# Optimization experiments

Hardware: AMD Instinct MI355X
Metric: run time of the kernel (lower is better)

Reference implementation:

```python
import jax, jax.numpy as jnp
import numpy as np

N_NODES = 50000
N_EDGES = 800000
N_GRAPHS = 2000
N_PAIRS = 4096
IN_CH = 64
EMB = 128
HID = 256
OUT = 1


def gcn_conv(x, edge_index, W, b):
    # PyG GCNConv: h = x @ W^T, then D^{-1/2}(A+I)D^{-1/2} h + b
    h = x @ W.T                                  # [N, out]
    row, col = edge_index[0], edge_index[1]
    ones = jnp.ones((edge_index.shape[1],), h.dtype)
    deg = jax.ops.segment_sum(ones, col, num_segments=N_NODES) + 1.0  # self-loop
    dinv = jax.lax.rsqrt(deg)
    norm = dinv[row] * dinv[col]                 # [E]
    agg = jax.ops.segment_sum(h[row] * norm[:, None], col, num_segments=N_NODES)
    agg = agg + h * (1.0 / deg)[:, None]         # self-loop term (dinv[i]^2)
    return agg + b


def setup_inputs() -> dict:
    key = jax.random.key(0)
    ks = jax.random.split(key, 10)
    x = jax.random.normal(ks[0], (N_NODES, IN_CH), jnp.float32)
    edge_index = jax.random.randint(ks[1], (2, N_EDGES), 0, N_NODES, jnp.int64)
    batch = jnp.sort(jax.random.randint(ks[2], (N_NODES,), 0, N_GRAPHS, jnp.int64))
    drug_drug_batch = jax.random.randint(ks[3], (2, N_PAIRS), 0, N_GRAPHS, jnp.int64)

    def xavier(k, shape):
        fan_out, fan_in = shape
        lim = jnp.sqrt(6.0 / (fan_in + fan_out))
        return jax.random.uniform(k, shape, jnp.float32, -lim, lim)

    return {
        "x": x, "edge_index": edge_index, "batch": batch,
        "drug_drug_batch": drug_drug_batch,
        "conv1_w": xavier(ks[4], (EMB, IN_CH)), "conv1_b": jnp.zeros((EMB,), jnp.float32),
        "conv2_w": xavier(ks[5], (EMB, EMB)), "conv2_b": jnp.zeros((EMB,), jnp.float32),
        "reg1_w": xavier(ks[6], (HID, 2 * EMB)), "reg1_b": jnp.zeros((HID,), jnp.float32),
        "reg2_w": xavier(ks[7], (OUT, HID)), "reg2_b": jnp.zeros((OUT,), jnp.float32),
    }


def reference(x, edge_index, batch, drug_drug_batch,
              conv1_w, conv1_b, conv2_w, conv2_b,
              reg1_w, reg1_b, reg2_w, reg2_b):
    h = jax.nn.relu(gcn_conv(x, edge_index, conv1_w, conv1_b))
    h = jax.nn.relu(gcn_conv(h, edge_index, conv2_w, conv2_b))

    # scatter_mean readout over graphs
    gsum = jax.ops.segment_sum(h, batch, num_segments=N_GRAPHS)
    cnt = jax.ops.segment_sum(jnp.ones((N_NODES,), h.dtype), batch, num_segments=N_GRAPHS)
    graph_embeds = gsum / jnp.maximum(cnt, 1.0)[:, None]

    # quantize drug ids to dense graph indices (np.digitize on unique+1, as in source)
    dd = np.asarray(drug_drug_batch)
    bins = np.unique(dd.flatten()) + 1
    q = jnp.asarray(np.digitize(dd, bins))       # [2, P]

    pairs = jnp.concatenate([graph_embeds[q[0]], graph_embeds[q[1]]], axis=1)  # [P, 2*EMB]
    out = jax.nn.relu(pairs @ reg1_w.T + reg1_b)
    return out @ reg2_w.T + reg2_b
```

## Files before the change

### kernel.cpp

```cpp
#include <hip/hip_runtime.h>

#define N_NODES  50000
#define N_PAD    50048
#define N_EDGES  800000
#define N_GRAPHS 2000
#define N_PAIRS  4096
#define IN_CH    64
#define EMB      128
#define HID      256
#define PPB      16

__global__ void k_pre(const int* __restrict__ col, const int* __restrict__ batch,
                      const float* __restrict__ w1, const float* __restrict__ w2,
                      int* __restrict__ deg, int* __restrict__ pos_e, int* __restrict__ cnt,
                      float* __restrict__ wt1, float* __restrict__ wt2) {
    int e = blockIdx.x * 256 + threadIdx.x;
    if (e < N_EDGES) {
        int c = col[e];
        pos_e[e] = atomicAdd(&deg[c], 1);
    }
    if (e < N_NODES) atomicAdd(&cnt[batch[e]], 1);
    if (e < EMB * IN_CH) {
        int j = e / IN_CH, k = e % IN_CH;
        wt1[k * EMB + j] = w1[e];
    } else if (e < EMB * IN_CH + EMB * EMB) {
        int t = e - EMB * IN_CH;
        int j = t / EMB, k = t % EMB;
        wt2[k * EMB + j] = w2[t];
    }
}

__device__ inline int wave_incl_scan(int x, int lane) {
    #pragma unroll
    for (int off = 1; off < 64; off <<= 1) {
        int y = __shfl_up(x, off, 64);
        if (lane >= off) x += y;
    }
    return x;
}

__global__ void k_scan1(const int* __restrict__ in, int* __restrict__ part, int n) {
    __shared__ int ws[4];
    int i = blockIdx.x * 256 + threadIdx.x;
    int lane = threadIdx.x & 63, wid = threadIdx.x >> 6;
    int v = (i < n) ? in[i] : 0;
    int x = wave_incl_scan(v, lane);
    if (lane == 63) ws[wid] = x;
    __syncthreads();
    if (threadIdx.x == 0) part[blockIdx.x] = ws[0] + ws[1] + ws[2] + ws[3];
}

__global__ void k_scan2(int* __restrict__ part, int nb) {
    __shared__ int ws[4];
    int t = threadIdx.x, lane = t & 63, wid = t >> 6;
    int v = (t < nb) ? part[t] : 0;
    int x = wave_incl_scan(v, lane);
    if (lane == 63) ws[wid] = x;
    __syncthreads();
    int add = 0;
    for (int w = 0; w < wid; ++w) add += ws[w];
    if (t < nb) part[t] = x - v + add;
}

__global__ void k_scan3d(const int* __restrict__ in, const int* __restrict__ part,
                         int* __restrict__ off, float* __restrict__ dinv) {
    __shared__ int ws[4];
    int i = blockIdx.x * 256 + threadIdx.x;
    int lane = threadIdx.x & 63, wid = threadIdx.x >> 6;
    int v = (i < N_NODES) ? in[i] : 0;
    int x = wave_incl_scan(v, lane);
    if (lane == 63) ws[wid] = x;
    __syncthreads();
    int add = part[blockIdx.x];
    for (int w = 0; w < wid; ++w) add += ws[w];
    if (i < N_NODES) {
        off[i] = x - v + add;
        dinv[i] = 1.0f / sqrtf((float)(v + 1));
    }
    if (i == 0) off[N_NODES] = N_EDGES;
}

__global__ void k_fill_scale(const int* __restrict__ row, const int* __restrict__ col,
                             const int* __restrict__ pos_e, const int* __restrict__ off,
                             int* __restrict__ csr_row,
                             const float4* __restrict__ x, const float* __restrict__ dinv,
                             float4* __restrict__ xs) {
    int idx = blockIdx.x * 256 + threadIdx.x;
    if (idx < N_EDGES) {
        int c = col[idx];
        int p = pos_e[idx];
        csr_row[off[c] + p] = row[idx];
    } else {
        int i = idx - N_EDGES;
        int n = i >> 4;
        float d = dinv[n];
        float4 v = x[i];
        v.x *= d; v.y *= d; v.z *= d; v.w *= d;
        xs[i] = v;
    }
}

__device__ inline void f4add(float4& a, const float4 b) {
    a.x += b.x; a.y += b.y; a.z += b.z; a.w += b.w;
}

template <int C>
__global__ void k_gather8(const float4* __restrict__ hs, const int* __restrict__ csr_row,
                          const int* __restrict__ off, const float* __restrict__ dinv,
                          float4* __restrict__ out) {
    constexpr int L = C / 4;
    constexpr int NPB = 256 / L;
    int local = threadIdx.x / L;
    int c4 = threadIdx.x % L;
    int n = blockIdx.x * NPB + local;
    int s = off[n], e = off[n + 1];
    float4 acc = hs[n * L + c4];
    int i = s;
    for (; i + 8 <= e; i += 8) {
        int r0 = csr_row[i + 0], r1 = csr_row[i + 1], r2 = csr_row[i + 2], r3 = csr_row[i + 3];
        int r4 = csr_row[i + 4], r5 = csr_row[i + 5], r6 = csr_row[i + 6], r7 = csr_row[i + 7];
        float4 a0 = hs[r0 * L + c4], a1 = hs[r1 * L + c4];
        float4 a2 = hs[r2 * L + c4], a3 = hs[r3 * L + c4];
        float4 a4 = hs[r4 * L + c4], a5 = hs[r5 * L + c4];
        float4 a6 = hs[r6 * L + c4], a7 = hs[r7 * L + c4];
        f4add(a0, a1); f4add(a2, a3); f4add(a4, a5); f4add(a6, a7);
        f4add(a0, a2); f4add(a4, a6);
        f4add(a0, a4);
        f4add(acc, a0);
    }
    for (; i < e; ++i) {
        int r = csr_row[i];
        float4 a = hs[r * L + c4];
        f4add(acc, a);
    }
    float dn = dinv[n];
    acc.x *= dn; acc.y *= dn; acc.z *= dn; acc.w *= dn;
    out[n * L + c4] = acc;
}

__global__ void k_gather_ro(const float4* __restrict__ t2, const int* __restrict__ csr_row,
                            const int* __restrict__ off, const float* __restrict__ dinv,
                            const float* __restrict__ bias, const int* __restrict__ batch,
                            float* __restrict__ gsum) {
    constexpr int L = EMB / 4;
    constexpr int NPB = 8;
    __shared__ __align__(16) float hb[NPB][EMB];
    __shared__ int bg[NPB];
    int local = threadIdx.x >> 5;
    int c4 = threadIdx.x & 31;
    int n0 = blockIdx.x * NPB;
    int n = n0 + local;
    if (threadIdx.x < NPB) bg[threadIdx.x] = batch[n0 + threadIdx.x];
    int s = off[n], e = off[n + 1];
    float4 acc = t2[n * L + c4];
    int i = s;
    for (; i + 8 <= e; i += 8) {
        int r0 = csr_row[i + 0], r1 = csr_row[i + 1], r2 = csr_row[i + 2], r3 = csr_row[i + 3];
        int r4 = csr_row[i + 4], r5 = csr_row[i + 5], r6 = csr_row[i + 6], r7 = csr_row[i + 7];
        float4 a0 = t2[r0 * L + c4], a1 = t2[r1 * L + c4];
        float4 a2 = t2[r2 * L + c4], a3 = t2[r3 * L + c4];
        float4 a4 = t2[r4 * L + c4], a5 = t2[r5 * L + c4];
        float4 a6 = t2[r6 * L + c4], a7 = t2[r7 * L + c4];
        f4add(a0, a1); f4add(a2, a3); f4add(a4, a5); f4add(a6, a7);
        f4add(a0, a2); f4add(a4, a6);
        f4add(a0, a4);
        f4add(acc, a0);
    }
    for (; i < e; ++i) {
        int r = csr_row[i];
        float4 a = t2[r * L + c4];
        f4add(acc, a);
    }
    float dn = dinv[n];
    float4 b = reinterpret_cast<const float4*>(bias)[c4];
    acc.x = fmaxf(fmaf(acc.x, dn, b.x), 0.f);
    acc.y = fmaxf(fmaf(acc.y, dn, b.y), 0.f);
    acc.z = fmaxf(fmaf(acc.z, dn, b.z), 0.f);
    acc.w = fmaxf(fmaf(acc.w, dn, b.w), 0.f);
    *reinterpret_cast<float4*>(&hb[local][c4 * 4]) = acc;
    __syncthreads();
    int ch = threadIdx.x;
    if (ch < EMB) {
        int g = bg[0];
        float a = 0.f;
        #pragma unroll
        for (int j = 0; j < NPB; ++j) {
            int gj = bg[j];
            if (gj != g) { atomicAdd(&gsum[g * EMB + ch], a); a = 0.f; g = gj; }
            a += hb[j][ch];
        }
        atomicAdd(&gsum[g * EMB + ch], a);
    }
}

template <int K, bool RELU, bool BIAS, bool POSTSCALE>
__global__ void k_gemmv5(const float* __restrict__ A, const float* __restrict__ Wt,
                         const float* __restrict__ bias, const float* __restrict__ rowscale,
                         float* __restrict__ out) {
    __shared__ __align__(16) float a_lds[64 * K];
    int t = threadIdx.x;
    {
        const float4* Ag = reinterpret_cast<const float4*>(A + (size_t)blockIdx.x * 64 * K);
        float4* Al = reinterpret_cast<float4*>(a_lds);
        constexpr int NV = (64 * K) / (4 * 256);
        #pragma unroll
        for (int i = 0; i < NV; ++i) Al[t + i * 256] = Ag[t + i * 256];
    }
    __syncthreads();
    int cq = (t & 31) << 2;
    int rg = t >> 5;
    float4 acc[8];
    #pragma unroll
    for (int r = 0; r < 8; ++r) acc[r] = make_float4(0.f, 0.f, 0.f, 0.f);
    #pragma unroll 2
    for (int k = 0; k < K; k += 4) {
        float4 w0 = *reinterpret_cast<const float4*>(&Wt[(k + 0) * EMB + cq]);
        float4 w1 = *reinterpret_cast<const float4*>(&Wt[(k + 1) * EMB + cq]);
        float4 w2 = *reinterpret_cast<const float4*>(&Wt[(k + 2) * EMB + cq]);
        float4 w3 = *reinterpret_cast<const float4*>(&Wt[(k + 3) * EMB + cq]);
        #pragma unroll
        for (int r = 0; r < 8; ++r) {
            float4 a = *reinterpret_cast<const float4*>(&a_lds[(rg * 8 + r) * K + k]);
            acc[r].x = fmaf(a.x, w0.x, fmaf(a.y, w1.x, fmaf(a.z, w2.x, fmaf(a.w, w3.x, acc[r].x))));
            acc[r].y = fmaf(a.x, w0.y, fmaf(a.y, w1.y, fmaf(a.z, w2.y, fmaf(a.w, w3.y, acc[r].y))));
            acc[r].z = fmaf(a.x, w0.z, fmaf(a.y, w1.z, fmaf(a.z, w2.z, fmaf(a.w, w3.z, acc[r].z))));
            acc[r].w = fmaf(a.x, w0.w, fmaf(a.y, w1.w, fmaf(a.z, w2.w, fmaf(a.w, w3.w, acc[r].w))));
        }
    }
    int row0 = blockIdx.x * 64 + rg * 8;
    #pragma unroll
    for (int r = 0; r < 8; ++r) {
        int row = row0 + r;
        if (row < N_NODES) {
            float4 v = acc[r];
            if (BIAS) {
                float4 b = *reinterpret_cast<const float4*>(&bias[cq]);
                v.x += b.x; v.y += b.y; v.z += b.z; v.w += b.w;
            }
            if (RELU) {
                v.x = fmaxf(v.x, 0.f); v.y = fmaxf(v.y, 0.f);
                v.z = fmaxf(v.z, 0.f); v.w = fmaxf(v.w, 0.f);
            }
            if (POSTSCALE) {
                float sc = rowscale[row];
                v.x *= sc; v.y *= sc; v.z *= sc; v.w *= sc;
            }
            *reinterpret_cast<float4*>(&out[(size_t)row * EMB + cq]) = v;
        }
    }
}

__global__ void k_digitize(const int* __restrict__ dd, int* __restrict__ rankx) {
    __shared__ int pres[N_GRAPHS];
    __shared__ int ws[4];
    __shared__ int carry;
    int t = threadIdx.x, lane = t & 63, wid = t >> 6;
    for (int i = t; i < N_GRAPHS; i += 256) pres[i] = 0;
    __syncthreads();
    for (int i = t; i < 2 * N_PAIRS; i += 256) pres[dd[i]] = 1;
    if (t == 0) carry = 0;
    __syncthreads();
    for (int base = 0; base < N_GRAPHS; base += 256) {
        int i = base + t;
        int v = (i < N_GRAPHS) ? pres[i] : 0;
        int x = wave_incl_scan(v, lane);
        if (lane == 63) ws[wid] = x;
        __syncthreads();
        int add = carry;
        for (int w = 0; w < wid; ++w) add += ws[w];
        if (i < N_GRAPHS) rankx[i] = x - v + add;
        __syncthreads();
        if (t == 255) carry = add + x;
        __syncthreads();
    }
}

__global__ void k_mlp16(const float* __restrict__ gemb, const int* __restrict__ cnt,
                        const int* __restrict__ dd, const int* __restrict__ rankx,
                        const float* __restrict__ w1, const float* __restrict__ b1,
                        const float* __restrict__ w2, const float* __restrict__ b2,
                        float* __restrict__ out) {
    __shared__ __align__(16) float pv[PPB][2 * EMB];
    __shared__ float wpart[4][PPB];
    int p0 = blockIdx.x * PPB;
    int t = threadIdx.x;
    int lane = t & 63, wid = t >> 6;
    #pragma unroll
    for (int j = 0; j < PPB; ++j) {
        int p = p0 + j;
        if (t < EMB) {
            int ga = rankx[dd[p]];
            int ca = cnt[ga];
            float ra = 1.0f / (float)(ca > 1 ? ca : 1);
            pv[j][t] = gemb[ga * EMB + t] * ra;
        } else {
            int gb = rankx[dd[N_PAIRS + p]];
            int cb = cnt[gb];
            float rb = 1.0f / (float)(cb > 1 ? cb : 1);
            pv[j][t] = gemb[gb * EMB + (t - EMB)] * rb;
        }
    }
    __syncthreads();
    float acc[PPB];
    float bv = b1[t];
    #pragma unroll
    for (int j = 0; j < PPB; ++j) acc[j] = bv;
    const float4* wrow = reinterpret_cast<const float4*>(&w1[t * 2 * EMB]);
    for (int k = 0; k < (2 * EMB) / 4; ++k) {
        float4 w = wrow[k];
        #pragma unroll
        for (int j = 0; j < PPB; ++j) {
            const float4 xv = *reinterpret_cast<const float4*>(&pv[j][k * 4]);
            acc[j] = fmaf(xv.x, w.x, fmaf(xv.y, w.y, fmaf(xv.z, w.z, fmaf(xv.w, w.w, acc[j]))));
        }
    }
    float w2t = w2[t];
    float contrib[PPB];
    #pragma unroll
    for (int j = 0; j < PPB; ++j) contrib[j] = fmaxf(acc[j], 0.f) * w2t;
    #pragma unroll
    for (int off = 32; off > 0; off >>= 1) {
        #pragma unroll
        for (int j = 0; j < PPB; ++j) contrib[j] += __shfl_down(contrib[j], off, 64);
    }
    if (lane == 0) {
        #pragma unroll
        for (int j = 0; j < PPB; ++j) wpart[wid][j] = contrib[j];
    }
    __syncthreads();
    if (t < PPB) {
        out[p0 + t] = wpart[0][t] + wpart[1][t] + wpart[2][t] + wpart[3][t] + b2[0];
    }
}

extern "C" void kernel_launch(void* const* d_in, const int* in_sizes, int n_in,
                              void* d_out, int out_size, void* d_ws, size_t ws_size,
                              hipStream_t stream) {
    const float* x        = (const float*)d_in[0];
    const int*   ei       = (const int*)d_in[1];
    const int*   batch    = (const int*)d_in[2];
    const int*   dd       = (const int*)d_in[3];
    const float* conv1_w  = (const float*)d_in[4];
    const float* conv1_b  = (const float*)d_in[5];
    const float* conv2_w  = (const float*)d_in[6];
    const float* conv2_b  = (const float*)d_in[7];
    const float* reg1_w   = (const float*)d_in[8];
    const float* reg1_b   = (const float*)d_in[9];
    const float* reg2_w   = (const float*)d_in[10];
    const float* reg2_b   = (const float*)d_in[11];
    float* outp = (float*)d_out;

    const int* ei_row = ei;
    const int* ei_col = ei + N_EDGES;

    char* ws = (char*)d_ws;
    size_t o = 0;
    auto alloc = [&](size_t bytes) -> void* {
        void* p = ws + o;
        o = (o + bytes + 255) & ~(size_t)255;
        return p;
    };
    size_t zero_start = o;
    int*   deg     = (int*)alloc(N_NODES * 4);
    int*   cnt     = (int*)alloc(N_GRAPHS * 4);
    float* gsum    = (float*)alloc(N_GRAPHS * EMB * 4);
    size_t zero_bytes = o - zero_start;
    int*   off     = (int*)alloc((N_NODES + 1) * 4);
    float* dinv    = (float*)alloc(N_NODES * 4);
    int*   part    = (int*)alloc(256 * 4);
    int*   pos_e   = (int*)alloc(N_EDGES * 4);
    int*   csr_row = (int*)alloc(N_EDGES * 4);
    int*   rankx   = (int*)alloc(N_GRAPHS * 4);
    float* Wt1     = (float*)alloc(IN_CH * EMB * 4);
    float* Wt2     = (float*)alloc(EMB * EMB * 4);
    float* aggx    = (float*)alloc((size_t)N_PAD * IN_CH * 4);
    float* h1s     = (float*)alloc((size_t)N_PAD * EMB * 4);
    float* t2      = (float*)alloc((size_t)N_PAD * EMB * 4);
    float* xs      = t2;

    (void)ws_size; (void)in_sizes; (void)n_in; (void)out_size;

    hipMemsetAsync(ws + zero_start, 0, zero_bytes, stream);

    k_pre<<<N_EDGES / 256, 256, 0, stream>>>(ei_col, batch, conv1_w, conv2_w,
                                             deg, pos_e, cnt, Wt1, Wt2);
    {
        int nb = (N_NODES + 255) / 256;
        k_scan1<<<nb, 256, 0, stream>>>(deg, part, N_NODES);
        k_scan2<<<1, 256, 0, stream>>>(part, nb);
        k_scan3d<<<nb, 256, 0, stream>>>(deg, part, off, dinv);
    }
    k_fill_scale<<<(N_EDGES + N_NODES * (IN_CH / 4)) / 256, 256, 0, stream>>>(
        ei_row, ei_col, pos_e, off, csr_row, (const float4*)x, dinv, (float4*)xs);

    k_gather8<IN_CH><<<N_NODES / (256 / (IN_CH / 4)), 256, 0, stream>>>(
        (const float4*)xs, csr_row, off, dinv, (float4*)aggx);
    k_gemmv5<IN_CH, true, true, true><<<N_PAD / 64, 256, 0, stream>>>(
        aggx, Wt1, conv1_b, dinv, h1s);

    k_gemmv5<EMB, false, false, false><<<N_PAD / 64, 256, 0, stream>>>(
        h1s, Wt2, nullptr, nullptr, t2);
    k_gather_ro<<<N_NODES / 8, 256, 0, stream>>>(
        (const float4*)t2, csr_row, off, dinv, conv2_b, batch, gsum);

    k_digitize<<<1, 256, 0, stream>>>(dd, rankx);

    k_mlp16<<<N_PAIRS / PPB, 256, 0, stream>>>(gsum, cnt, dd, rankx,
                                               reg1_w, reg1_b, reg2_w, reg2_b, outp);
}
```

Before: 238.9 us.

## Fuse conv1 gather into GEMM and split conv2 readout gather into channel halves

Conv1's neighbor aggregation is fused with the 64->128 GEMM in one kernel, so the intermediate aggx buffer is no longer written and re-read. The conv2 gather+readout is split into two launches, each covering 64 of the 128 channels. This halves the per-pass gather working set, likely for better cache hit rates, at the cost of reading the CSR indices twice. The fused kernel uses 32-node tiles with 4 rows per thread, which lowers arithmetic reuse of the weights per block.

```diff
diff --git a/kernel.cpp b/kernel.cpp
--- a/kernel.cpp
+++ b/kernel.cpp
@@ -104,98 +104,87 @@
     a.x += b.x; a.y += b.y; a.z += b.z; a.w += b.w;
 }
 
-template <int C>
-__global__ void k_gather8(const float4* __restrict__ hs, const int* __restrict__ csr_row,
-                          const int* __restrict__ off, const float* __restrict__ dinv,
-                          float4* __restrict__ out) {
-    constexpr int L = C / 4;
-    constexpr int NPB = 256 / L;
-    int local = threadIdx.x / L;
-    int c4 = threadIdx.x % L;
-    int n = blockIdx.x * NPB + local;
-    int s = off[n], e = off[n + 1];
-    float4 acc = hs[n * L + c4];
-    int i = s;
-    for (; i + 8 <= e; i += 8) {
-        int r0 = csr_row[i + 0], r1 = csr_row[i + 1], r2 = csr_row[i + 2], r3 = csr_row[i + 3];
-        int r4 = csr_row[i + 4], r5 = csr_row[i + 5], r6 = csr_row[i + 6], r7 = csr_row[i + 7];
-        float4 a0 = hs[r0 * L + c4], a1 = hs[r1 * L + c4];
-        float4 a2 = hs[r2 * L + c4], a3 = hs[r3 * L + c4];
-        float4 a4 = hs[r4 * L + c4], a5 = hs[r5 * L + c4];
-        float4 a6 = hs[r6 * L + c4], a7 = hs[r7 * L + c4];
-        f4add(a0, a1); f4add(a2, a3); f4add(a4, a5); f4add(a6, a7);
-        f4add(a0, a2); f4add(a4, a6);
-        f4add(a0, a4);
-        f4add(acc, a0);
-    }
-    for (; i < e; ++i) {
-        int r = csr_row[i];
-        float4 a = hs[r * L + c4];
-        f4add(acc, a);
-    }
-    float dn = dinv[n];
-    acc.x *= dn; acc.y *= dn; acc.z *= dn; acc.w *= dn;
-    out[n * L + c4] = acc;
-}
-
-__global__ void k_gather_ro(const float4* __restrict__ t2, const int* __restrict__ csr_row,
-                            const int* __restrict__ off, const float* __restrict__ dinv,
-                            const float* __restrict__ bias, const int* __restrict__ batch,
-                            float* __restrict__ gsum) {
-    constexpr int L = EMB / 4;
-    constexpr int NPB = 8;
-    __shared__ __align__(16) float hb[NPB][EMB];
-    __shared__ int bg[NPB];
-    int local = threadIdx.x >> 5;
-    int c4 = threadIdx.x & 31;
-    int n0 = blockIdx.x * NPB;
-    int n = n0 + local;
-    if (threadIdx.x < NPB) bg[threadIdx.x] = batch[n0 + threadIdx.x];
-    int s = off[n], e = off[n + 1];
-    float4 acc = t2[n * L + c4];
-    int i = s;
-    for (; i + 8 <= e; i += 8) {
-        int r0 = csr_row[i + 0], r1 = csr_row[i + 1], r2 = csr_row[i + 2], r3 = csr_row[i + 3];
-        int r4 = csr_row[i + 4], r5 = csr_row[i + 5], r6 = csr_row[i + 6], r7 = csr_row[i + 7];
-        float4 a0 = t2[r0 * L + c4], a1 = t2[r1 * L + c4];
-        float4 a2 = t2[r2 * L + c4], a3 = t2[r3 * L + c4];
-        float4 a4 = t2[r4 * L + c4], a5 = t2[r5 * L + c4];
-        float4 a6 = t2[r6 * L + c4], a7 = t2[r7 * L + c4];
-        f4add(a0, a1); f4add(a2, a3); f4add(a4, a5); f4add(a6, a7);
-        f4add(a0, a2); f4add(a4, a6);
-        f4add(a0, a4);
-        f4add(acc, a0);
-    }
-    for (; i < e; ++i) {
-        int r = csr_row[i];
-        float4 a = t2[r * L + c4];
-        f4add(acc, a);
-    }
-    float dn = dinv[n];
-    float4 b = reinterpret_cast<const float4*>(bias)[c4];
-    acc.x = fmaxf(fmaf(acc.x, dn, b.x), 0.f);
-    acc.y = fmaxf(fmaf(acc.y, dn, b.y), 0.f);
-    acc.z = fmaxf(fmaf(acc.z, dn, b.z), 0.f);
-    acc.w = fmaxf(fmaf(acc.w, dn, b.w), 0.f);
-    *reinterpret_cast<float4*>(&hb[local][c4 * 4]) = acc;
-    __syncthreads();
-    int ch = threadIdx.x;
-    if (ch < EMB) {
-        int g = bg[0];
-        float a = 0.f;
-        #pragma unroll
-        for (int j = 0; j < NPB; ++j) {
-            int gj = bg[j];
-            if (gj != g) { atomicAdd(&gsum[g * EMB + ch], a); a = 0.f; g = gj; }
-            a += hb[j][ch];
-        }
-        atomicAdd(&gsum[g * EMB + ch], a);
-    }
-}
-
-template <int K, bool RELU, bool BIAS, bool POSTSCALE>
+__global__ __launch_bounds__(256) void k_conv1f(
+        const float4* __restrict__ xs, const int* __restrict__ csr_row,
+        const int* __restrict__ off, const float* __restrict__ dinv,
+        const float* __restrict__ w1t, const float* __restrict__ b1,
+        float* __restrict__ h1s) {
+    __shared__ __align__(16) float a_lds[32 * IN_CH];
+    int t = threadIdx.x;
+    int base = blockIdx.x * 32;
+    {
+        int c4 = t & 15;
+        #pragma unroll
+        for (int g = 0; g < 2; ++g) {
+            int nl = (t >> 4) + g * 16;
+            int n = base + nl;
+            float4 acc = make_float4(0.f, 0.f, 0.f, 0.f);
+            if (n < N_NODES) {
+                int s = off[n], e = off[n + 1];
+                acc = xs[n * 16 + c4];
+                int i = s;
+                for (; i + 8 <= e; i += 8) {
+                    int r0 = csr_row[i + 0], r1 = csr_row[i + 1], r2 = csr_row[i + 2], r3 = csr_row[i + 3];
+                    int r4 = csr_row[i + 4], r5 = csr_row[i + 5], r6 = csr_row[i + 6], r7 = csr_row[i + 7];
+                    float4 a0 = xs[r0 * 16 + c4], a1 = xs[r1 * 16 + c4];
+                    float4 a2 = xs[r2 * 16 + c4], a3 = xs[r3 * 16 + c4];
+                    float4 a4 = xs[r4 * 16 + c4], a5 = xs[r5 * 16 + c4];
+                    float4 a6 = xs[r6 * 16 + c4], a7 = xs[r7 * 16 + c4];
+                    f4add(a0, a1); f4add(a2, a3); f4add(a4, a5); f4add(a6, a7);
+                    f4add(a0, a2); f4add(a4, a6);
+                    f4add(a0, a4);
+                    f4add(acc, a0);
+                }
+                for (; i < e; ++i) {
+                    float4 a = xs[csr_row[i] * 16 + c4];
+                    f4add(acc, a);
+                }
+                float dn = dinv[n];
+                acc.x *= dn; acc.y *= dn; acc.z *= dn; acc.w *= dn;
+            }
+            *reinterpret_cast<float4*>(&a_lds[nl * IN_CH + c4 * 4]) = acc;
+        }
+    }
+    __syncthreads();
+    {
+        int cq = (t & 31) << 2;
+        int rg = t >> 5;
+        float4 acc[4];
+        #pragma unroll
+        for (int r = 0; r < 4; ++r) acc[r] = make_float4(0.f, 0.f, 0.f, 0.f);
+        #pragma unroll 2
+        for (int k = 0; k < IN_CH; k += 4) {
+            float4 w0 = *reinterpret_cast<const float4*>(&w1t[(k + 0) * EMB + cq]);
+            float4 w1 = *reinterpret_cast<const float4*>(&w1t[(k + 1) * EMB + cq]);
+            float4 w2 = *reinterpret_cast<const float4*>(&w1t[(k + 2) * EMB + cq]);
+            float4 w3 = *reinterpret_cast<const float4*>(&w1t[(k + 3) * EMB + cq]);
+            #pragma unroll
+            for (int r = 0; r < 4; ++r) {
+                float4 a = *reinterpret_cast<const float4*>(&a_lds[(rg * 4 + r) * IN_CH + k]);
+                acc[r].x = fmaf(a.x, w0.x, fmaf(a.y, w1.x, fmaf(a.z, w2.x, fmaf(a.w, w3.x, acc[r].x))));
+                acc[r].y = fmaf(a.x, w0.y, fmaf(a.y, w1.y, fmaf(a.z, w2.y, fmaf(a.w, w3.y, acc[r].y))));
+                acc[r].z = fmaf(a.x, w0.z, fmaf(a.y, w1.z, fmaf(a.z, w2.z, fmaf(a.w, w3.z, acc[r].z))));
+                acc[r].w = fmaf(a.x, w0.w, fmaf(a.y, w1.w, fmaf(a.z, w2.w, fmaf(a.w, w3.w, acc[r].w))));
+            }
+        }
+        float4 bv = *reinterpret_cast<const float4*>(&b1[cq]);
+        #pragma unroll
+        for (int r = 0; r < 4; ++r) {
+            int row = base + rg * 4 + r;
+            if (row < N_NODES) {
+                float4 v = acc[r];
+                v.x += bv.x; v.y += bv.y; v.z += bv.z; v.w += bv.w;
+                float sc = dinv[row];
+                v.x = fmaxf(v.x, 0.f) * sc; v.y = fmaxf(v.y, 0.f) * sc;
+                v.z = fmaxf(v.z, 0.f) * sc; v.w = fmaxf(v.w, 0.f) * sc;
+                *reinterpret_cast<float4*>(&h1s[(size_t)row * EMB + cq]) = v;
+            }
+        }
+    }
+}
+
+template <int K>
 __global__ void k_gemmv5(const float* __restrict__ A, const float* __restrict__ Wt,
-                         const float* __restrict__ bias, const float* __restrict__ rowscale,
                          float* __restrict__ out) {
     __shared__ __align__(16) float a_lds[64 * K];
     int t = threadIdx.x;
@@ -232,21 +221,65 @@
     for (int r = 0; r < 8; ++r) {
         int row = row0 + r;
         if (row < N_NODES) {
-            float4 v = acc[r];
-            if (BIAS) {
-                float4 b = *reinterpret_cast<const float4*>(&bias[cq]);
-                v.x += b.x; v.y += b.y; v.z += b.z; v.w += b.w;
-            }
-            if (RELU) {
-                v.x = fmaxf(v.x, 0.f); v.y = fmaxf(v.y, 0.f);
-                v.z = fmaxf(v.z, 0.f); v.w = fmaxf(v.w, 0.f);
-            }
-            if (POSTSCALE) {
-                float sc = rowscale[row];
-                v.x *= sc; v.y *= sc; v.z *= sc; v.w *= sc;
-            }
-            *reinterpret_cast<float4*>(&out[(size_t)row * EMB + cq]) = v;
-        }
+            *reinterpret_cast<float4*>(&out[(size_t)row * EMB + cq]) = acc[r];
+        }
+    }
+}
+
+template <int HALF>
+__global__ void k_gro_h(const float4* __restrict__ t2, const int* __restrict__ csr_row,
+                        const int* __restrict__ off, const float* __restrict__ dinv,
+                        const float* __restrict__ bias, const int* __restrict__ batch,
+                        float* __restrict__ gsum) {
+    constexpr int NPB = 16;
+    __shared__ __align__(16) float hb[NPB][64];
+    __shared__ int bg[NPB];
+    int t = threadIdx.x;
+    int local = t >> 4;
+    int c4 = t & 15;
+    int n0 = blockIdx.x * NPB;
+    int n = n0 + local;
+    if (t < NPB) bg[t] = batch[n0 + t];
+    int s = off[n], e = off[n + 1];
+    const int cidx = HALF * 16 + c4;
+    float4 acc = t2[(size_t)n * 32 + cidx];
+    int i = s;
+    for (; i + 8 <= e; i += 8) {
+        int r0 = csr_row[i + 0], r1 = csr_row[i + 1], r2 = csr_row[i + 2], r3 = csr_row[i + 3];
+        int r4 = csr_row[i + 4], r5 = csr_row[i + 5], r6 = csr_row[i + 6], r7 = csr_row[i + 7];
+        float4 a0 = t2[(size_t)r0 * 32 + cidx], a1 = t2[(size_t)r1 * 32 + cidx];
+        float4 a2 = t2[(size_t)r2 * 32 + cidx], a3 = t2[(size_t)r3 * 32 + cidx];
+        float4 a4 = t2[(size_t)r4 * 32 + cidx], a5 = t2[(size_t)r5 * 32 + cidx];
+        float4 a6 = t2[(size_t)r6 * 32 + cidx], a7 = t2[(size_t)r7 * 32 + cidx];
+        f4add(a0, a1); f4add(a2, a3); f4add(a4, a5); f4add(a6, a7);
+        f4add(a0, a2); f4add(a4, a6);
+        f4add(a0, a4);
+        f4add(acc, a0);
+    }
+    for (; i < e; ++i) {
+        float4 a = t2[(size_t)csr_row[i] * 32 + cidx];
+        f4add(acc, a);
+    }
+    float dn = dinv[n];
+    float4 b = reinterpret_cast<const float4*>(bias)[cidx];
+    acc.x = fmaxf(fmaf(acc.x, dn, b.x), 0.f);
+    acc.y = fmaxf(fmaf(acc.y, dn, b.y), 0.f);
+    acc.z = fmaxf(fmaf(acc.z, dn, b.z), 0.f);
+    acc.w = fmaxf(fmaf(acc.w, dn, b.w), 0.f);
+    *reinterpret_cast<float4*>(&hb[local][c4 * 4]) = acc;
+    __syncthreads();
+    {
+        int ch = t & 63, q = t >> 6;
+        int j0 = q * 4;
+        int g = bg[j0];
+        float a = 0.f;
+        #pragma unroll
+        for (int j = j0; j < j0 + 4; ++j) {
+            int gj = bg[j];
+            if (gj != g) { atomicAdd(&gsum[g * EMB + HALF * 64 + ch], a); a = 0.f; g = gj; }
+            a += hb[j][ch];
+        }
+        atomicAdd(&gsum[g * EMB + HALF * 64 + ch], a);
     }
 }
 
@@ -373,7 +406,6 @@
     int*   rankx   = (int*)alloc(N_GRAPHS * 4);
     float* Wt1     = (float*)alloc(IN_CH * EMB * 4);
     float* Wt2     = (float*)alloc(EMB * EMB * 4);
-    float* aggx    = (float*)alloc((size_t)N_PAD * IN_CH * 4);
     float* h1s     = (float*)alloc((size_t)N_PAD * EMB * 4);
     float* t2      = (float*)alloc((size_t)N_PAD * EMB * 4);
     float* xs      = t2;
@@ -393,14 +425,13 @@
     k_fill_scale<<<(N_EDGES + N_NODES * (IN_CH / 4)) / 256, 256, 0, stream>>>(
         ei_row, ei_col, pos_e, off, csr_row, (const float4*)x, dinv, (float4*)xs);
 
-    k_gather8<IN_CH><<<N_NODES / (256 / (IN_CH / 4)), 256, 0, stream>>>(
-        (const float4*)xs, csr_row, off, dinv, (float4*)aggx);
-    k_gemmv5<IN_CH, true, true, true><<<N_PAD / 64, 256, 0, stream>>>(
-        aggx, Wt1, conv1_b, dinv, h1s);
-
-    k_gemmv5<EMB, false, false, false><<<N_PAD / 64, 256, 0, stream>>>(
-        h1s, Wt2, nullptr, nullptr, t2);
-    k_gather_ro<<<N_NODES / 8, 256, 0, stream>>>(
+    k_conv1f<<<N_PAD / 32, 256, 0, stream>>>(
+        (const float4*)xs, csr_row, off, dinv, Wt1, conv1_b, h1s);
+
+    k_gemmv5<EMB><<<N_PAD / 64, 256, 0, stream>>>(h1s, Wt2, t2);
+    k_gro_h<0><<<N_NODES / 16, 256, 0, stream>>>(
+        (const float4*)t2, csr_row, off, dinv, conv2_b, batch, gsum);
+    k_gro_h<1><<<N_NODES / 16, 256, 0, stream>>>(
         (const float4*)t2, csr_row, off, dinv, conv2_b, batch, gsum);
 
     k_digitize<<<1, 256, 0, stream>>>(dd, rankx);
```

New measurement: 236.8 us. Within noise of the previous version (-0.9%).

## Split layer-2 gather-readout into channel halves and fold digitize into scan2

Applied to the files above, without the earlier changes.

The layer-2 gather plus readout now runs as two launches, each covering 64 of the 128 channels with 16 nodes per block. Each pass therefore touches a smaller slice of t2, which should improve cache hit rates for the random neighbor gathers. The separate single-block digitize kernel is merged into the scan2 launch as a second block, removing one tiny launch from the serial chain. In exchange the CSR indices, offsets and per-node metadata are read twice, and the readout issues more atomics.

```diff
diff --git a/kernel.cpp b/kernel.cpp
--- a/kernel.cpp
+++ b/kernel.cpp
@@ -50,16 +50,41 @@
     if (threadIdx.x == 0) part[blockIdx.x] = ws[0] + ws[1] + ws[2] + ws[3];
 }
 
-__global__ void k_scan2(int* __restrict__ part, int nb) {
-    __shared__ int ws[4];
+__global__ void k_scan2d(int* __restrict__ part, int nb,
+                         const int* __restrict__ dd, int* __restrict__ rankx) {
     int t = threadIdx.x, lane = t & 63, wid = t >> 6;
-    int v = (t < nb) ? part[t] : 0;
-    int x = wave_incl_scan(v, lane);
-    if (lane == 63) ws[wid] = x;
-    __syncthreads();
-    int add = 0;
-    for (int w = 0; w < wid; ++w) add += ws[w];
-    if (t < nb) part[t] = x - v + add;
+    if (blockIdx.x == 0) {
+        __shared__ int ws[4];
+        int v = (t < nb) ? part[t] : 0;
+        int x = wave_incl_scan(v, lane);
+        if (lane == 63) ws[wid] = x;
+        __syncthreads();
+        int add = 0;
+        for (int w = 0; w < wid; ++w) add += ws[w];
+        if (t < nb) part[t] = x - v + add;
+    } else {
+        __shared__ int pres[N_GRAPHS];
+        __shared__ int ws2[4];
+        __shared__ int carry;
+        for (int i = t; i < N_GRAPHS; i += 256) pres[i] = 0;
+        __syncthreads();
+        for (int i = t; i < 2 * N_PAIRS; i += 256) pres[dd[i]] = 1;
+        if (t == 0) carry = 0;
+        __syncthreads();
+        for (int base = 0; base < N_GRAPHS; base += 256) {
+            int i = base + t;
+            int v = (i < N_GRAPHS) ? pres[i] : 0;
+            int x = wave_incl_scan(v, lane);
+            if (lane == 63) ws2[wid] = x;
+            __syncthreads();
+            int add = carry;
+            for (int w = 0; w < wid; ++w) add += ws2[w];
+            if (i < N_GRAPHS) rankx[i] = x - v + add;
+            __syncthreads();
+            if (t == 255) carry = add + x;
+            __syncthreads();
+        }
+    }
 }
 
 __global__ void k_scan3d(const int* __restrict__ in, const int* __restrict__ part,
@@ -138,61 +163,6 @@
     out[n * L + c4] = acc;
 }
 
-__global__ void k_gather_ro(const float4* __restrict__ t2, const int* __restrict__ csr_row,
-                            const int* __restrict__ off, const float* __restrict__ dinv,
-                            const float* __restrict__ bias, const int* __restrict__ batch,
-                            float* __restrict__ gsum) {
-    constexpr int L = EMB / 4;
-    constexpr int NPB = 8;
-    __shared__ __align__(16) float hb[NPB][EMB];
-    __shared__ int bg[NPB];
-    int local = threadIdx.x >> 5;
-    int c4 = threadIdx.x & 31;
-    int n0 = blockIdx.x * NPB;
-    int n = n0 + local;
-    if (threadIdx.x < NPB) bg[threadIdx.x] = batch[n0 + threadIdx.x];
-    int s = off[n], e = off[n + 1];
-    float4 acc = t2[n * L + c4];
-    int i = s;
-    for (; i + 8 <= e; i += 8) {
-        int r0 = csr_row[i + 0], r1 = csr_row[i + 1], r2 = csr_row[i + 2], r3 = csr_row[i + 3];
-        int r4 = csr_row[i + 4], r5 = csr_row[i + 5], r6 = csr_row[i + 6], r7 = csr_row[i + 7];
-        float4 a0 = t2[r0 * L + c4], a1 = t2[r1 * L + c4];
-        float4 a2 = t2[r2 * L + c4], a3 = t2[r3 * L + c4];
-        float4 a4 = t2[r4 * L + c4], a5 = t2[r5 * L + c4];
-        float4 a6 = t2[r6 * L + c4], a7 = t2[r7 * L + c4];
-        f4add(a0, a1); f4add(a2, a3); f4add(a4, a5); f4add(a6, a7);
-        f4add(a0, a2); f4add(a4, a6);
-        f4add(a0, a4);
-        f4add(acc, a0);
-    }
-    for (; i < e; ++i) {
-        int r = csr_row[i];
-        float4 a = t2[r * L + c4];
-        f4add(acc, a);
-    }
-    float dn = dinv[n];
-    float4 b = reinterpret_cast<const float4*>(bias)[c4];
-    acc.x = fmaxf(fmaf(acc.x, dn, b.x), 0.f);
-    acc.y = fmaxf(fmaf(acc.y, dn, b.y), 0.f);
-    acc.z = fmaxf(fmaf(acc.z, dn, b.z), 0.f);
-    acc.w = fmaxf(fmaf(acc.w, dn, b.w), 0.f);
-    *reinterpret_cast<float4*>(&hb[local][c4 * 4]) = acc;
-    __syncthreads();
-    int ch = threadIdx.x;
-    if (ch < EMB) {
-        int g = bg[0];
-        float a = 0.f;
-        #pragma unroll
-        for (int j = 0; j < NPB; ++j) {
-            int gj = bg[j];
-            if (gj != g) { atomicAdd(&gsum[g * EMB + ch], a); a = 0.f; g = gj; }
-            a += hb[j][ch];
-        }
-        atomicAdd(&gsum[g * EMB + ch], a);
-    }
-}
-
 template <int K, bool RELU, bool BIAS, bool POSTSCALE>
 __global__ void k_gemmv5(const float* __restrict__ A, const float* __restrict__ Wt,
                          const float* __restrict__ bias, const float* __restrict__ rowscale,
@@ -250,28 +220,60 @@
     }
 }
 
-__global__ void k_digitize(const int* __restrict__ dd, int* __restrict__ rankx) {
-    __shared__ int pres[N_GRAPHS];
-    __shared__ int ws[4];
-    __shared__ int carry;
-    int t = threadIdx.x, lane = t & 63, wid = t >> 6;
-    for (int i = t; i < N_GRAPHS; i += 256) pres[i] = 0;
-    __syncthreads();
-    for (int i = t; i < 2 * N_PAIRS; i += 256) pres[dd[i]] = 1;
-    if (t == 0) carry = 0;
-    __syncthreads();
-    for (int base = 0; base < N_GRAPHS; base += 256) {
-        int i = base + t;
-        int v = (i < N_GRAPHS) ? pres[i] : 0;
-        int x = wave_incl_scan(v, lane);
-        if (lane == 63) ws[wid] = x;
-        __syncthreads();
-        int add = carry;
-        for (int w = 0; w < wid; ++w) add += ws[w];
-        if (i < N_GRAPHS) rankx[i] = x - v + add;
-        __syncthreads();
-        if (t == 255) carry = add + x;
-        __syncthreads();
+template <int HALF>
+__global__ void k_gro_h(const float4* __restrict__ t2, const int* __restrict__ csr_row,
+                        const int* __restrict__ off, const float* __restrict__ dinv,
+                        const float* __restrict__ bias, const int* __restrict__ batch,
+                        float* __restrict__ gsum) {
+    constexpr int NPB = 16;
+    __shared__ __align__(16) float hb[NPB][64];
+    __shared__ int bg[NPB];
+    int t = threadIdx.x;
+    int local = t >> 4;
+    int c4 = t & 15;
+    int n0 = blockIdx.x * NPB;
+    int n = n0 + local;
+    if (t < NPB) bg[t] = batch[n0 + t];
+    int s = off[n], e = off[n + 1];
+    const int cidx = HALF * 16 + c4;
+    float4 acc = t2[(size_t)n * 32 + cidx];
+    int i = s;
+    for (; i + 8 <= e; i += 8) {
+        int r0 = csr_row[i + 0], r1 = csr_row[i + 1], r2 = csr_row[i + 2], r3 = csr_row[i + 3];
+        int r4 = csr_row[i + 4], r5 = csr_row[i + 5], r6 = csr_row[i + 6], r7 = csr_row[i + 7];
+        float4 a0 = t2[(size_t)r0 * 32 + cidx], a1 = t2[(size_t)r1 * 32 + cidx];
+        float4 a2 = t2[(size_t)r2 * 32 + cidx], a3 = t2[(size_t)r3 * 32 + cidx];
+        float4 a4 = t2[(size_t)r4 * 32 + cidx], a5 = t2[(size_t)r5 * 32 + cidx];
+        float4 a6 = t2[(size_t)r6 * 32 + cidx], a7 = t2[(size_t)r7 * 32 + cidx];
+        f4add(a0, a1); f4add(a2, a3); f4add(a4, a5); f4add(a6, a7);
+        f4add(a0, a2); f4add(a4, a6);
+        f4add(a0, a4);
+        f4add(acc, a0);
+    }
+    for (; i < e; ++i) {
+        float4 a = t2[(size_t)csr_row[i] * 32 + cidx];
+        f4add(acc, a);
+    }
+    float dn = dinv[n];
+    float4 b = reinterpret_cast<const float4*>(bias)[cidx];
+    acc.x = fmaxf(fmaf(acc.x, dn, b.x), 0.f);
+    acc.y = fmaxf(fmaf(acc.y, dn, b.y), 0.f);
+    acc.z = fmaxf(fmaf(acc.z, dn, b.z), 0.f);
+    acc.w = fmaxf(fmaf(acc.w, dn, b.w), 0.f);
+    *reinterpret_cast<float4*>(&hb[local][c4 * 4]) = acc;
+    __syncthreads();
+    {
+        int ch = t & 63, q = t >> 6;
+        int j0 = q * 4;
+        int g = bg[j0];
+        float a = 0.f;
+        #pragma unroll
+        for (int j = j0; j < j0 + 4; ++j) {
+            int gj = bg[j];
+            if (gj != g) { atomicAdd(&gsum[g * EMB + HALF * 64 + ch], a); a = 0.f; g = gj; }
+            a += hb[j][ch];
+        }
+        atomicAdd(&gsum[g * EMB + HALF * 64 + ch], a);
     }
 }
 
@@ -387,7 +389,7 @@
     {
         int nb = (N_NODES + 255) / 256;
         k_scan1<<<nb, 256, 0, stream>>>(deg, part, N_NODES);
-        k_scan2<<<1, 256, 0, stream>>>(part, nb);
+        k_scan2d<<<2, 256, 0, stream>>>(part, nb, dd, rankx);
         k_scan3d<<<nb, 256, 0, stream>>>(deg, part, off, dinv);
     }
     k_fill_scale<<<(N_EDGES + N_NODES * (IN_CH / 4)) / 256, 256, 0, stream>>>(
@@ -400,10 +402,10 @@
 
     k_gemmv5<EMB, false, false, false><<<N_PAD / 64, 256, 0, stream>>>(
         h1s, Wt2, nullptr, nullptr, t2);
-    k_gather_ro<<<N_NODES / 8, 256, 0, stream>>>(
+    k_gro_h<0><<<N_NODES / 16, 256, 0, stream>>>(
         (const float4*)t2, csr_row, off, dinv, conv2_b, batch, gsum);
-
-    k_digitize<<<1, 256, 0, stream>>>(dd, rankx);
+    k_gro_h<1><<<N_NODES / 16, 256, 0, stream>>>(
+        (const float4*)t2, csr_row, off, dinv, conv2_b, batch, gsum);
 
     k_mlp16<<<N_PAIRS / PPB, 256, 0, stream>>>(gsum, cnt, dd, rankx,
                                                reg1_w, reg1_b, reg2_w, reg2_b, outp);
```

Result: no change. 240.1 us (+0.5%).
